# Optimization experiments

Hardware: AMD Instinct MI355X
Metric: run time of the kernel (lower is better)

The kernel has to match this reference:

```python
import jax, jax.numpy as jnp
import numpy as np

NUM_HEADS = 32
NUM_KV_HEADS = 8
HEAD_DIM = 128
HIDDEN = 4096
BLOCK_SIZE = 16
NUM_BLOCKS = 512
BLOCKS_PER_REQ = 256
B, S = 1, 2048
ROPE_BASE = 10000.0


def _rope_cos_sin(seq_len, dim, dtype):
    inv_freq = 1.0 / (ROPE_BASE ** (jnp.arange(0, dim, 2, dtype=jnp.float32) / dim))
    t = jnp.arange(seq_len, dtype=jnp.float32)
    freqs = jnp.outer(t, inv_freq)            # [S, dim/2]
    emb = jnp.concatenate([freqs, freqs], -1)  # [S, dim]
    return jnp.cos(emb).astype(dtype), jnp.sin(emb).astype(dtype)


def _rotate_half(x):
    d = x.shape[-1] // 2
    return jnp.concatenate([-x[..., d:], x[..., :d]], axis=-1)


def setup_inputs() -> dict:
    key = jax.random.key(0)
    ks = jax.random.split(key, 6)
    sc = 0.02
    return {
        "hidden_states": jax.random.normal(ks[0], (B, S, HIDDEN), jnp.float32),
        "k_cache": jax.random.normal(ks[1], (NUM_BLOCKS, NUM_KV_HEADS, BLOCK_SIZE, HEAD_DIM), jnp.float32),
        "v_cache": jax.random.normal(ks[2], (NUM_BLOCKS, NUM_KV_HEADS, BLOCK_SIZE, HEAD_DIM), jnp.float32),
        "Wq": jax.random.normal(ks[3], (HIDDEN, HIDDEN), jnp.float32) * sc,
        "Wo": jax.random.normal(ks[4], (HIDDEN, HIDDEN), jnp.float32) * sc,
        "block_table": jax.random.randint(ks[5], (BLOCKS_PER_REQ,), 0, NUM_BLOCKS, jnp.int32),
    }


def reference(hidden_states, k_cache, v_cache, Wq, Wo, block_table):
    Bq, Sq, D = hidden_states.shape
    # query projection + reshape to [B, H, S, d]
    q = (hidden_states @ Wq.T).reshape(Bq, Sq, NUM_HEADS, HEAD_DIM).transpose(0, 2, 1, 3)
    cos, sin = _rope_cos_sin(Sq, HEAD_DIM, q.dtype)  # [S, d]
    q = q * cos[None, None] + _rotate_half(q) * sin[None, None]

    # paged KV gather: [n_blk, kvH, blk, d] -> [kvH, kv_len, d]
    kv_len = BLOCKS_PER_REQ * BLOCK_SIZE
    K = k_cache[block_table].transpose(1, 0, 2, 3).reshape(NUM_KV_HEADS, kv_len, HEAD_DIM)
    V = v_cache[block_table].transpose(1, 0, 2, 3).reshape(NUM_KV_HEADS, kv_len, HEAD_DIM)

    # GQA: repeat_interleave kv heads to q heads
    factor = NUM_HEADS // NUM_KV_HEADS
    K = jnp.repeat(K, factor, axis=0)[None]  # [1, H, kv_len, d]
    V = jnp.repeat(V, factor, axis=0)[None]

    scores = jnp.einsum('bhsd,bhkd->bhsk', q, K) / jnp.sqrt(jnp.asarray(HEAD_DIM, q.dtype))
    attn = jax.nn.softmax(scores, axis=-1)
    ctx = jnp.einsum('bhsk,bhkd->bhsd', attn, V)
    ctx = ctx.transpose(0, 2, 1, 3).reshape(Bq, Sq, D)
    return ctx @ Wo.T
```

## Files before the change

### kernel.cpp

```cpp
#include <hip/hip_runtime.h>
#include <hip/hip_bf16.h>

typedef __bf16 bf16;
typedef __bf16 bf16x4 __attribute__((ext_vector_type(4)));
typedef __bf16 bf16x8 __attribute__((ext_vector_type(8)));
typedef float f32x4 __attribute__((ext_vector_type(4)));

#define AS1 __attribute__((address_space(1)))
#define AS3 __attribute__((address_space(3)))
#define GLD16(gptr, lptr) \
  __builtin_amdgcn_global_load_lds((const AS1 unsigned int*)(gptr), \
                                   (AS3 unsigned int*)(lptr), 16, 0, 0)

#define NUM_H   32
#define NUM_KVH 8
#define DH      128
#define SEQ     2048
#define KVLEN   4096
#define HID     4096
#define RSCALE  0.08838834764831845f

__global__ void prep_hs(const float* __restrict__ hs, bf16* __restrict__ out) {
  int tid = blockIdx.x * 256 + threadIdx.x;
  size_t o = (size_t)tid * 8;
  float4 a = *(const float4*)(hs + o);
  float4 b = *(const float4*)(hs + o + 4);
  bf16x8 w = {(bf16)a.x, (bf16)a.y, (bf16)a.z, (bf16)a.w,
              (bf16)b.x, (bf16)b.y, (bf16)b.z, (bf16)b.w};
  *(bf16x8*)(out + o) = w;
}

__global__ void prep_k(const float* __restrict__ kc, const int* __restrict__ bt,
                       bf16* __restrict__ Kg) {
  int tid = blockIdx.x * 256 + threadIdx.x;
  int c   = tid & 31;
  int j   = (tid >> 5) & 4095;
  int kvh = tid >> 17;
  int blk = bt[j >> 4];
  float4 v = *(const float4*)(kc + (((size_t)blk * NUM_KVH + kvh) * 16 + (j & 15)) * DH + c * 4);
  bf16x4 w = {(bf16)v.x, (bf16)v.y, (bf16)v.z, (bf16)v.w};
  *(bf16x4*)(Kg + ((size_t)kvh * KVLEN + j) * DH + c * 4) = w;
}

__global__ void prep_v(const float* __restrict__ vc, const int* __restrict__ bt,
                       bf16* __restrict__ Vt) {
  __shared__ bf16 T[32][136];
  int e2 = blockIdx.x & 127, kvh = blockIdx.x >> 7;
  int t = threadIdx.x;
#pragma unroll
  for (int i = 0; i < 4; i++) {
    int idx = i * 256 + t;
    int pg  = idx >> 9;
    int pos = (idx >> 5) & 15;
    int c4  = idx & 31;
    int blk = bt[e2 * 2 + pg];
    float4 v = *(const float4*)(vc + (((size_t)blk * NUM_KVH + kvh) * 16 + pos) * DH + c4 * 4);
    bf16x4 w = {(bf16)v.x, (bf16)v.y, (bf16)v.z, (bf16)v.w};
    *(bf16x4*)(&T[pg * 16 + pos][c4 * 4]) = w;
  }
  __syncthreads();
  int d = t & 127, jc = t >> 7;
  bf16 tmp[16];
#pragma unroll
  for (int j = 0; j < 16; j++) tmp[j] = T[jc * 16 + j][d];
  bf16* dst = Vt + ((size_t)kvh * DH + d) * KVLEN + e2 * 32 + jc * 16;
  *(bf16x8*)dst = *(bf16x8*)tmp;
  *(bf16x8*)(dst + 8) = *(bf16x8*)(tmp + 8);
}

template <typename CT>
__global__ __launch_bounds__(512, 2)
void gemm_bb(const bf16* __restrict__ A, const bf16* __restrict__ B,
             CT* __restrict__ C, int M, int N, int K) {
  __shared__ alignas(16) bf16 As[2][128 * 64];
  __shared__ alignas(16) bf16 Bs[2][256 * 64];
  const int nwg = gridDim.x;
  const int q8  = nwg >> 3;
  const int wg  = ((int)blockIdx.x & 7) * q8 + ((int)blockIdx.x >> 3);
  const int nb = N >> 8;
  const int bm = wg / nb;
  const int bn = wg % nb;
  const int t = threadIdx.x;
  const int lane = t & 63, wave = t >> 6;
  const int lid = lane & 15, quad = lane >> 4;
  const int wm = (wave >> 2) * 64, wn = (wave & 3) * 64;
  const bf16* Ab = A + (size_t)bm * 128 * K;
  const bf16* Bb = B + (size_t)bn * 256 * K;
  f32x4 acc[4][4] = {};

  auto stage = [&](int buf, int k0) {
#pragma unroll
    for (int i = 0; i < 2; i++) {
      int id = i * 512 + t;
      int row = id >> 3, c = id & 7;
      int gc = c ^ (row & 7);
      GLD16(Ab + (size_t)row * K + k0 + gc * 8, &As[buf][id * 8]);
    }
#pragma unroll
    for (int i = 0; i < 4; i++) {
      int id = i * 512 + t;
      int row = id >> 3, c = id & 7;
      int gc = c ^ (row & 7);
      GLD16(Bb + (size_t)row * K + k0 + gc * 8, &Bs[buf][id * 8]);
    }
  };
  auto compute = [&](int buf) {
#pragma unroll
    for (int kk = 0; kk < 2; kk++) {
      bf16x8 af[4], bfr[4];
#pragma unroll
      for (int i = 0; i < 4; i++) {
        int row = wm + i * 16 + lid;
        af[i] = *(const bf16x8*)(&As[buf][row * 64 + ((kk * 4 + quad) ^ (row & 7)) * 8]);
      }
#pragma unroll
      for (int j = 0; j < 4; j++) {
        int row = wn + j * 16 + lid;
        bfr[j] = *(const bf16x8*)(&Bs[buf][row * 64 + ((kk * 4 + quad) ^ (row & 7)) * 8]);
      }
#pragma unroll
      for (int i = 0; i < 4; i++)
#pragma unroll
        for (int j = 0; j < 4; j++)
          acc[i][j] = __builtin_amdgcn_mfma_f32_16x16x32_bf16(af[i], bfr[j], acc[i][j], 0, 0, 0);
    }
  };

  stage(0, 0);
  __syncthreads();

  int cur = 0;
#pragma unroll 1
  for (int k0 = 64; k0 < K; k0 += 64) {
    stage(cur ^ 1, k0);
    __builtin_amdgcn_sched_barrier(0);
    compute(cur);
    __syncthreads();
    cur ^= 1;
  }
  compute(cur);

#pragma unroll
  for (int i = 0; i < 4; i++)
#pragma unroll
    for (int j = 0; j < 4; j++)
#pragma unroll
      for (int r = 0; r < 4; r++) {
        int m = bm * 128 + wm + i * 16 + quad * 4 + r;
        int n = bn * 256 + wn + j * 16 + lid;
        C[(size_t)m * N + n] = (CT)acc[i][j][r];
      }
}

template <typename CT>
__global__ __launch_bounds__(512, 2)
void gemm_bt2(const bf16* __restrict__ A, const float* __restrict__ B,
              CT* __restrict__ C, int M, int N, int K) {
  __shared__ alignas(16) bf16 As[2][128 * 64];
  __shared__ alignas(16) bf16 Bs[2][256 * 64];
  const int nb = N >> 8;
  const int bm = (int)blockIdx.x / nb;
  const int bn = (int)blockIdx.x % nb;
  const int t = threadIdx.x;
  const int lane = t & 63, wave = t >> 6;
  const int lid = lane & 15, quad = lane >> 4;
  const int wm = (wave >> 2) * 64, wn = (wave & 3) * 64;
  const bf16*  Ab = A + (size_t)bm * 128 * K;
  const float* Bb = B + (size_t)bn * 256 * K;
  f32x4 acc[4][4] = {};
  float4 breg[4][2];

  auto issueA = [&](int buf, int k0) {
#pragma unroll
    for (int i = 0; i < 2; i++) {
      int id = i * 512 + t;
      int row = id >> 3, c = id & 7;
      int gc = c ^ (row & 7);
      GLD16(Ab + (size_t)row * K + k0 + gc * 8, &As[buf][id * 8]);
    }
  };
  auto loadB = [&](int k0) {
#pragma unroll
    for (int i = 0; i < 4; i++) {
      int id = i * 512 + t;
      int row = id >> 3, c = id & 7;
      const float* src = Bb + (size_t)row * K + k0 + c * 8;
      breg[i][0] = *(const float4*)(src);
      breg[i][1] = *(const float4*)(src + 4);
    }
  };
  auto writeB = [&](int buf) {
#pragma unroll
    for (int i = 0; i < 4; i++) {
      int id = i * 512 + t;
      int row = id >> 3, c = id & 7;
      int sc = c ^ (row & 7);
      float4 u = breg[i][0], v = breg[i][1];
      bf16x8 w = {(bf16)u.x, (bf16)u.y, (bf16)u.z, (bf16)u.w,
                  (bf16)v.x, (bf16)v.y, (bf16)v.z, (bf16)v.w};
      *(bf16x8*)(&Bs[buf][row * 64 + sc * 8]) = w;
    }
  };
  auto compute = [&](int buf) {
#pragma unroll
    for (int kk = 0; kk < 2; kk++) {
      bf16x8 af[4], bfr[4];
#pragma unroll
      for (int i = 0; i < 4; i++) {
        int row = wm + i * 16 + lid;
        af[i] = *(const bf16x8*)(&As[buf][row * 64 + ((kk * 4 + quad) ^ (row & 7)) * 8]);
      }
#pragma unroll
      for (int j = 0; j < 4; j++) {
        int row = wn + j * 16 + lid;
        bfr[j] = *(const bf16x8*)(&Bs[buf][row * 64 + ((kk * 4 + quad) ^ (row & 7)) * 8]);
      }
#pragma unroll
      for (int i = 0; i < 4; i++)
#pragma unroll
        for (int j = 0; j < 4; j++)
          acc[i][j] = __builtin_amdgcn_mfma_f32_16x16x32_bf16(af[i], bfr[j], acc[i][j], 0, 0, 0);
    }
  };

  issueA(0, 0);
  loadB(0);
  writeB(0);
  __syncthreads();

  int cur = 0;
#pragma unroll 1
  for (int k0 = 64; k0 < K; k0 += 64) {
    issueA(cur ^ 1, k0);
    loadB(k0);
    __builtin_amdgcn_sched_barrier(0);
    compute(cur);
    __builtin_amdgcn_sched_barrier(0);
    writeB(cur ^ 1);
    __syncthreads();
    cur ^= 1;
  }
  compute(cur);

#pragma unroll
  for (int i = 0; i < 4; i++)
#pragma unroll
    for (int j = 0; j < 4; j++)
#pragma unroll
      for (int r = 0; r < 4; r++) {
        int m = bm * 128 + wm + i * 16 + quad * 4 + r;
        int n = bn * 256 + wn + j * 16 + lid;
        C[(size_t)m * N + n] = (CT)acc[i][j][r];
      }
}

__global__ void rope_q(bf16* __restrict__ Q) {
  __shared__ float tcs[64], tsn[64];
  int s = blockIdx.x;
  int t = threadIdx.x;
  if (t < 64) {
    float freq = expf(-(float)t * (logf(10000.f) / 64.f));
    float sn, cs;
    sincosf((float)s * freq, &sn, &cs);
    tsn[t] = sn; tcs[t] = cs;
  }
  __syncthreads();
  int h = t >> 3, d0 = (t & 7) * 8;
  bf16* ptr = Q + (size_t)s * HID + h * DH;
  bf16x8 lo = *(bf16x8*)(ptr + d0);
  bf16x8 hi = *(bf16x8*)(ptr + 64 + d0);
  bf16x8 olo, ohi;
#pragma unroll
  for (int e = 0; e < 8; e++) {
    float cs = tcs[d0 + e], sn = tsn[d0 + e];
    float q0 = (float)lo[e], q1 = (float)hi[e];
    olo[e] = (bf16)((q0 * cs - q1 * sn) * RSCALE);
    ohi[e] = (bf16)((q1 * cs + q0 * sn) * RSCALE);
  }
  *(bf16x8*)(ptr + d0) = olo;
  *(bf16x8*)(ptr + 64 + d0) = ohi;
}

__global__ __launch_bounds__(256, 2)
void attn(bf16* __restrict__ Q,
          const bf16* __restrict__ Kg,
          const bf16* __restrict__ Vt) {
  __shared__ alignas(16) bf16 Ks[64 * 128];
  __shared__ alignas(16) bf16 Vs[128 * 64];
  __shared__ alignas(16) bf16 Ps[4][2][16 * 72];
  const int bid = ((int)blockIdx.x & 7) * 64 + ((int)blockIdx.x >> 3);
  const int h = bid >> 4, qt2 = bid & 15;
  const int kvh = h >> 2;
  const int t = threadIdx.x;
  const int wave = t >> 6, lane = t & 63;
  const int lid = lane & 15, quad = lane >> 4;

  bf16x8 qf[2][4];
#pragma unroll
  for (int x = 0; x < 2; x++) {
    const bf16* qb = Q + (size_t)(qt2 * 128 + x * 64 + wave * 16 + lid) * HID + h * DH;
#pragma unroll
    for (int kc = 0; kc < 4; kc++) qf[x][kc] = *(const bf16x8*)(qb + kc * 32 + quad * 8);
  }
  const bf16* Kh = Kg + (size_t)kvh * KVLEN * DH;
  const bf16* Vh = Vt + (size_t)kvh * DH * KVLEN;
  f32x4 acc_o[2][8] = {};
  f32x4 lsum[2] = {};
  const bf16 one = (bf16)1.0f;
  const bf16x8 ones = {one, one, one, one, one, one, one, one};

  for (int kv0 = 0; kv0 < KVLEN; kv0 += 64) {
    __syncthreads();
#pragma unroll
    for (int i = 0; i < 4; i++) {
      int id = i * 256 + t;
      int row = id >> 4, cs = id & 15;
      int gc = cs ^ (row & 7);
      GLD16(Kh + (size_t)(kv0 + row) * DH + gc * 8, Ks + id * 8);
    }
#pragma unroll
    for (int i = 0; i < 4; i++) {
      int id = i * 256 + t;
      int d = id >> 3, cs = id & 7;
      int gc = cs ^ (d & 7);
      GLD16(Vh + (size_t)d * KVLEN + kv0 + gc * 8, Vs + id * 8);
    }
    __syncthreads();

    f32x4 sv[2][4];
#pragma unroll
    for (int n = 0; n < 4; n++) {
      f32x4 s0 = {}, s1 = {};
      int row = n * 16 + lid;
#pragma unroll
      for (int kc = 0; kc < 4; kc++) {
        int cs = (kc * 4 + quad) ^ (row & 7);
        bf16x8 kf = *(const bf16x8*)(Ks + row * DH + cs * 8);
        s0 = __builtin_amdgcn_mfma_f32_16x16x32_bf16(qf[0][kc], kf, s0, 0, 0, 0);
        s1 = __builtin_amdgcn_mfma_f32_16x16x32_bf16(qf[1][kc], kf, s1, 0, 0, 0);
      }
      sv[0][n] = s0; sv[1][n] = s1;
    }

#pragma unroll
    for (int x = 0; x < 2; x++)
#pragma unroll
      for (int r = 0; r < 4; r++)
#pragma unroll
        for (int n = 0; n < 4; n++)
          Ps[wave][x][(quad * 4 + r) * 72 + n * 16 + lid] = (bf16)__expf(sv[x][n][r]);

    bf16x8 pf[2][2];
#pragma unroll
    for (int x = 0; x < 2; x++)
#pragma unroll
      for (int kvc = 0; kvc < 2; kvc++)
        pf[x][kvc] = *(const bf16x8*)(&Ps[wave][x][0] + lid * 72 + kvc * 32 + quad * 8);

#pragma unroll
    for (int x = 0; x < 2; x++) {
      lsum[x] = __builtin_amdgcn_mfma_f32_16x16x32_bf16(pf[x][0], ones, lsum[x], 0, 0, 0);
      lsum[x] = __builtin_amdgcn_mfma_f32_16x16x32_bf16(pf[x][1], ones, lsum[x], 0, 0, 0);
    }

#pragma unroll
    for (int dt = 0; dt < 8; dt++) {
      int d = dt * 16 + lid;
#pragma unroll
      for (int kvc = 0; kvc < 2; kvc++) {
        int cs = (kvc * 4 + quad) ^ (d & 7);
        bf16x8 vf = *(const bf16x8*)(Vs + d * 64 + cs * 8);
        acc_o[0][dt] = __builtin_amdgcn_mfma_f32_16x16x32_bf16(pf[0][kvc], vf, acc_o[0][dt], 0, 0, 0);
        acc_o[1][dt] = __builtin_amdgcn_mfma_f32_16x16x32_bf16(pf[1][kvc], vf, acc_o[1][dt], 0, 0, 0);
      }
    }
  }

#pragma unroll
  for (int x = 0; x < 2; x++) {
    float rinv[4];
#pragma unroll
    for (int r = 0; r < 4; r++) rinv[r] = 1.0f / lsum[x][r];
#pragma unroll
    for (int dt = 0; dt < 8; dt++)
#pragma unroll
      for (int r = 0; r < 4; r++) {
        int m = qt2 * 128 + x * 64 + wave * 16 + quad * 4 + r;
        Q[(size_t)m * HID + h * DH + dt * 16 + lid] = (bf16)(acc_o[x][dt][r] * rinv[r]);
      }
  }
}

extern "C" void kernel_launch(void* const* d_in, const int* in_sizes, int n_in,
                              void* d_out, int out_size, void* d_ws, size_t ws_size,
                              hipStream_t stream) {
  const float* hs  = (const float*)d_in[0];
  const float* kca = (const float*)d_in[1];
  const float* vca = (const float*)d_in[2];
  const float* Wq  = (const float*)d_in[3];
  const float* Wo  = (const float*)d_in[4];
  const int*   bt  = (const int*)d_in[5];
  float* out = (float*)d_out;

  bf16* Qlin  = (bf16*)d_ws;
  bf16* Kg    = (bf16*)d_out;
  bf16* Vt    = (bf16*)((char*)d_out + (8u << 20));
  bf16* hs_bf = (bf16*)((char*)d_out + (16u << 20));

  prep_k<<<4096, 256, 0, stream>>>(kca, bt, Kg);
  prep_v<<<1024, 256, 0, stream>>>(vca, bt, Vt);
  prep_hs<<<4096, 256, 0, stream>>>(hs, hs_bf);

  if (ws_size >= (80u << 20)) {
    bf16* Wq_bf = (bf16*)((char*)d_ws + (16u << 20));
    bf16* Wo_bf = (bf16*)((char*)d_ws + (48u << 20));
    prep_hs<<<8192, 256, 0, stream>>>(Wq, Wq_bf);
    prep_hs<<<8192, 256, 0, stream>>>(Wo, Wo_bf);
    gemm_bb<bf16><<<256, 512, 0, stream>>>(hs_bf, Wq_bf, Qlin, SEQ, HID, HID);
    rope_q<<<SEQ, 256, 0, stream>>>(Qlin);
    attn<<<512, 256, 0, stream>>>(Qlin, Kg, Vt);
    gemm_bb<float><<<256, 512, 0, stream>>>(Qlin, Wo_bf, out, SEQ, HID, HID);
  } else {
    gemm_bt2<bf16><<<256, 512, 0, stream>>>(hs_bf, Wq, Qlin, SEQ, HID, HID);
    rope_q<<<SEQ, 256, 0, stream>>>(Qlin);
    attn<<<512, 256, 0, stream>>>(Qlin, Kg, Vt);
    gemm_bt2<float><<<256, 512, 0, stream>>>(Qlin, Wo, out, SEQ, HID, HID);
  }
}
```

Measured before the change: 558.7 us.

## Shrink GEMM tiles, double-buffer attention KV, swap MFMA operands for vector stores

Result: faster. 522.9 us (-6.4%).

```diff
diff --git a/kernel.cpp b/kernel.cpp
--- a/kernel.cpp
+++ b/kernel.cpp
@@ -69,36 +69,36 @@
 }
 
 template <typename CT>
-__global__ __launch_bounds__(512, 2)
+__global__ __launch_bounds__(256, 2)
 void gemm_bb(const bf16* __restrict__ A, const bf16* __restrict__ B,
              CT* __restrict__ C, int M, int N, int K) {
   __shared__ alignas(16) bf16 As[2][128 * 64];
-  __shared__ alignas(16) bf16 Bs[2][256 * 64];
+  __shared__ alignas(16) bf16 Bs[2][128 * 64];
   const int nwg = gridDim.x;
   const int q8  = nwg >> 3;
   const int wg  = ((int)blockIdx.x & 7) * q8 + ((int)blockIdx.x >> 3);
-  const int nb = N >> 8;
+  const int nb = N >> 7;
   const int bm = wg / nb;
   const int bn = wg % nb;
   const int t = threadIdx.x;
   const int lane = t & 63, wave = t >> 6;
   const int lid = lane & 15, quad = lane >> 4;
-  const int wm = (wave >> 2) * 64, wn = (wave & 3) * 64;
+  const int wm = (wave >> 1) * 64, wn = (wave & 1) * 64;
   const bf16* Ab = A + (size_t)bm * 128 * K;
-  const bf16* Bb = B + (size_t)bn * 256 * K;
+  const bf16* Bb = B + (size_t)bn * 128 * K;
   f32x4 acc[4][4] = {};
 
   auto stage = [&](int buf, int k0) {
 #pragma unroll
-    for (int i = 0; i < 2; i++) {
-      int id = i * 512 + t;
+    for (int i = 0; i < 4; i++) {
+      int id = i * 256 + t;
       int row = id >> 3, c = id & 7;
       int gc = c ^ (row & 7);
       GLD16(Ab + (size_t)row * K + k0 + gc * 8, &As[buf][id * 8]);
     }
 #pragma unroll
     for (int i = 0; i < 4; i++) {
-      int id = i * 512 + t;
+      int id = i * 256 + t;
       int row = id >> 3, c = id & 7;
       int gc = c ^ (row & 7);
       GLD16(Bb + (size_t)row * K + k0 + gc * 8, &Bs[buf][id * 8]);
@@ -122,7 +122,7 @@
       for (int i = 0; i < 4; i++)
 #pragma unroll
         for (int j = 0; j < 4; j++)
-          acc[i][j] = __builtin_amdgcn_mfma_f32_16x16x32_bf16(af[i], bfr[j], acc[i][j], 0, 0, 0);
+          acc[i][j] = __builtin_amdgcn_mfma_f32_16x16x32_bf16(bfr[j], af[i], acc[i][j], 0, 0, 0);
     }
   };
 
@@ -143,13 +143,168 @@
 #pragma unroll
   for (int i = 0; i < 4; i++)
 #pragma unroll
-    for (int j = 0; j < 4; j++)
-#pragma unroll
-      for (int r = 0; r < 4; r++) {
-        int m = bm * 128 + wm + i * 16 + quad * 4 + r;
-        int n = bn * 256 + wn + j * 16 + lid;
-        C[(size_t)m * N + n] = (CT)acc[i][j][r];
-      }
+    for (int j = 0; j < 4; j++) {
+      int m = bm * 128 + wm + i * 16 + lid;
+      int n = bn * 128 + wn + j * 16 + quad * 4;
+      if constexpr (sizeof(CT) == 4) {
+        float4 w = {acc[i][j][0], acc[i][j][1], acc[i][j][2], acc[i][j][3]};
+        *(float4*)(&C[(size_t)m * N + n]) = w;
+      } else {
+        bf16x4 w = {(bf16)acc[i][j][0], (bf16)acc[i][j][1],
+                    (bf16)acc[i][j][2], (bf16)acc[i][j][3]};
+        *(bf16x4*)(&C[(size_t)m * N + n]) = w;
+      }
+    }
+}
+
+__global__ void rope_q(bf16* __restrict__ Q) {
+  __shared__ float tcs[64], tsn[64];
+  int s = blockIdx.x;
+  int t = threadIdx.x;
+  if (t < 64) {
+    float freq = expf(-(float)t * (logf(10000.f) / 64.f));
+    float sn, cs;
+    sincosf((float)s * freq, &sn, &cs);
+    tsn[t] = sn; tcs[t] = cs;
+  }
+  __syncthreads();
+  int h = t >> 3, d0 = (t & 7) * 8;
+  bf16* ptr = Q + (size_t)s * HID + h * DH;
+  bf16x8 lo = *(bf16x8*)(ptr + d0);
+  bf16x8 hi = *(bf16x8*)(ptr + 64 + d0);
+  bf16x8 olo, ohi;
+#pragma unroll
+  for (int e = 0; e < 8; e++) {
+    float cs = tcs[d0 + e], sn = tsn[d0 + e];
+    float q0 = (float)lo[e], q1 = (float)hi[e];
+    olo[e] = (bf16)((q0 * cs - q1 * sn) * RSCALE);
+    ohi[e] = (bf16)((q1 * cs + q0 * sn) * RSCALE);
+  }
+  *(bf16x8*)(ptr + d0) = olo;
+  *(bf16x8*)(ptr + 64 + d0) = ohi;
+}
+
+__global__ __launch_bounds__(256, 2)
+void attn(bf16* __restrict__ Q,
+          const bf16* __restrict__ Kg,
+          const bf16* __restrict__ Vt) {
+  __shared__ alignas(16) bf16 Ks[2][64 * 128];
+  __shared__ alignas(16) bf16 Vs[2][128 * 64];
+  __shared__ alignas(16) bf16 Ps[4][2][1024];
+  const int bid = ((int)blockIdx.x & 7) * 64 + ((int)blockIdx.x >> 3);
+  const int h = bid >> 4, qt2 = bid & 15;
+  const int kvh = h >> 2;
+  const int t = threadIdx.x;
+  const int wave = t >> 6, lane = t & 63;
+  const int lid = lane & 15, quad = lane >> 4;
+
+  bf16x8 qf[2][4];
+#pragma unroll
+  for (int x = 0; x < 2; x++) {
+    const bf16* qb = Q + (size_t)(qt2 * 128 + x * 64 + wave * 16 + lid) * HID + h * DH;
+#pragma unroll
+    for (int kc = 0; kc < 4; kc++) qf[x][kc] = *(const bf16x8*)(qb + kc * 32 + quad * 8);
+  }
+  const bf16* Kh = Kg + (size_t)kvh * KVLEN * DH;
+  const bf16* Vh = Vt + (size_t)kvh * DH * KVLEN;
+  f32x4 acc_o[2][8] = {};
+  f32x4 lsum[2] = {};
+  const bf16 one = (bf16)1.0f;
+  const bf16x8 ones = {one, one, one, one, one, one, one, one};
+
+  auto stage = [&](int buf, int kv0) {
+#pragma unroll
+    for (int i = 0; i < 4; i++) {
+      int id = i * 256 + t;
+      int row = id >> 4, cs = id & 15;
+      int gc = cs ^ (row & 7);
+      GLD16(Kh + (size_t)(kv0 + row) * DH + gc * 8, &Ks[buf][id * 8]);
+    }
+#pragma unroll
+    for (int i = 0; i < 4; i++) {
+      int id = i * 256 + t;
+      int d = id >> 3, cs = id & 7;
+      int gc = cs ^ (d & 7);
+      GLD16(Vh + (size_t)d * KVLEN + kv0 + gc * 8, &Vs[buf][id * 8]);
+    }
+  };
+
+  stage(0, 0);
+  __syncthreads();
+
+  int cur = 0;
+#pragma unroll 1
+  for (int kv0 = 0; kv0 < KVLEN; kv0 += 64) {
+    if (kv0 + 64 < KVLEN) stage(cur ^ 1, kv0 + 64);
+    __builtin_amdgcn_sched_barrier(0);
+
+    f32x4 sv[2][4];
+#pragma unroll
+    for (int n = 0; n < 4; n++) {
+      f32x4 s0 = {}, s1 = {};
+      int row = n * 16 + lid;
+#pragma unroll
+      for (int kc = 0; kc < 4; kc++) {
+        int cs = (kc * 4 + quad) ^ (row & 7);
+        bf16x8 kf = *(const bf16x8*)(&Ks[cur][row * DH + cs * 8]);
+        s0 = __builtin_amdgcn_mfma_f32_16x16x32_bf16(kf, qf[0][kc], s0, 0, 0, 0);
+        s1 = __builtin_amdgcn_mfma_f32_16x16x32_bf16(kf, qf[1][kc], s1, 0, 0, 0);
+      }
+      sv[0][n] = s0; sv[1][n] = s1;
+    }
+
+#pragma unroll
+    for (int x = 0; x < 2; x++)
+#pragma unroll
+      for (int n = 0; n < 4; n++) {
+        bf16x4 w = {(bf16)__expf(sv[x][n][0]), (bf16)__expf(sv[x][n][1]),
+                    (bf16)__expf(sv[x][n][2]), (bf16)__expf(sv[x][n][3])};
+        int c = (2 * n + (quad >> 1)) ^ (lid & 7);
+        *(bf16x4*)(&Ps[wave][x][lid * 64 + c * 8 + (quad & 1) * 4]) = w;
+      }
+
+    bf16x8 pf[2][2];
+#pragma unroll
+    for (int x = 0; x < 2; x++)
+#pragma unroll
+      for (int kvc = 0; kvc < 2; kvc++) {
+        int c = (kvc * 4 + quad) ^ (lid & 7);
+        pf[x][kvc] = *(const bf16x8*)(&Ps[wave][x][lid * 64 + c * 8]);
+      }
+
+#pragma unroll
+    for (int x = 0; x < 2; x++) {
+      lsum[x] = __builtin_amdgcn_mfma_f32_16x16x32_bf16(ones, pf[x][0], lsum[x], 0, 0, 0);
+      lsum[x] = __builtin_amdgcn_mfma_f32_16x16x32_bf16(ones, pf[x][1], lsum[x], 0, 0, 0);
+    }
+
+#pragma unroll
+    for (int dt = 0; dt < 8; dt++) {
+      int d = dt * 16 + lid;
+#pragma unroll
+      for (int kvc = 0; kvc < 2; kvc++) {
+        int cs = (kvc * 4 + quad) ^ (d & 7);
+        bf16x8 vf = *(const bf16x8*)(&Vs[cur][d * 64 + cs * 8]);
+        acc_o[0][dt] = __builtin_amdgcn_mfma_f32_16x16x32_bf16(vf, pf[0][kvc], acc_o[0][dt], 0, 0, 0);
+        acc_o[1][dt] = __builtin_amdgcn_mfma_f32_16x16x32_bf16(vf, pf[1][kvc], acc_o[1][dt], 0, 0, 0);
+      }
+    }
+
+    __syncthreads();
+    cur ^= 1;
+  }
+
+#pragma unroll
+  for (int x = 0; x < 2; x++) {
+    float rinv = 1.0f / lsum[x][0];
+    int q = qt2 * 128 + x * 64 + wave * 16 + lid;
+#pragma unroll
+    for (int dt = 0; dt < 8; dt++) {
+      bf16x4 w = {(bf16)(acc_o[x][dt][0] * rinv), (bf16)(acc_o[x][dt][1] * rinv),
+                  (bf16)(acc_o[x][dt][2] * rinv), (bf16)(acc_o[x][dt][3] * rinv)};
+      *(bf16x4*)(&Q[(size_t)q * HID + h * DH + dt * 16 + quad * 4]) = w;
+    }
+  }
 }
 
 template <typename CT>
@@ -254,143 +409,6 @@
       }
 }
 
-__global__ void rope_q(bf16* __restrict__ Q) {
-  __shared__ float tcs[64], tsn[64];
-  int s = blockIdx.x;
-  int t = threadIdx.x;
-  if (t < 64) {
-    float freq = expf(-(float)t * (logf(10000.f) / 64.f));
-    float sn, cs;
-    sincosf((float)s * freq, &sn, &cs);
-    tsn[t] = sn; tcs[t] = cs;
-  }
-  __syncthreads();
-  int h = t >> 3, d0 = (t & 7) * 8;
-  bf16* ptr = Q + (size_t)s * HID + h * DH;
-  bf16x8 lo = *(bf16x8*)(ptr + d0);
-  bf16x8 hi = *(bf16x8*)(ptr + 64 + d0);
-  bf16x8 olo, ohi;
-#pragma unroll
-  for (int e = 0; e < 8; e++) {
-    float cs = tcs[d0 + e], sn = tsn[d0 + e];
-    float q0 = (float)lo[e], q1 = (float)hi[e];
-    olo[e] = (bf16)((q0 * cs - q1 * sn) * RSCALE);
-    ohi[e] = (bf16)((q1 * cs + q0 * sn) * RSCALE);
-  }
-  *(bf16x8*)(ptr + d0) = olo;
-  *(bf16x8*)(ptr + 64 + d0) = ohi;
-}
-
-__global__ __launch_bounds__(256, 2)
-void attn(bf16* __restrict__ Q,
-          const bf16* __restrict__ Kg,
-          const bf16* __restrict__ Vt) {
-  __shared__ alignas(16) bf16 Ks[64 * 128];
-  __shared__ alignas(16) bf16 Vs[128 * 64];
-  __shared__ alignas(16) bf16 Ps[4][2][16 * 72];
-  const int bid = ((int)blockIdx.x & 7) * 64 + ((int)blockIdx.x >> 3);
-  const int h = bid >> 4, qt2 = bid & 15;
-  const int kvh = h >> 2;
-  const int t = threadIdx.x;
-  const int wave = t >> 6, lane = t & 63;
-  const int lid = lane & 15, quad = lane >> 4;
-
-  bf16x8 qf[2][4];
-#pragma unroll
-  for (int x = 0; x < 2; x++) {
-    const bf16* qb = Q + (size_t)(qt2 * 128 + x * 64 + wave * 16 + lid) * HID + h * DH;
-#pragma unroll
-    for (int kc = 0; kc < 4; kc++) qf[x][kc] = *(const bf16x8*)(qb + kc * 32 + quad * 8);
-  }
-  const bf16* Kh = Kg + (size_t)kvh * KVLEN * DH;
-  const bf16* Vh = Vt + (size_t)kvh * DH * KVLEN;
-  f32x4 acc_o[2][8] = {};
-  f32x4 lsum[2] = {};
-  const bf16 one = (bf16)1.0f;
-  const bf16x8 ones = {one, one, one, one, one, one, one, one};
-
-  for (int kv0 = 0; kv0 < KVLEN; kv0 += 64) {
-    __syncthreads();
-#pragma unroll
-    for (int i = 0; i < 4; i++) {
-      int id = i * 256 + t;
-      int row = id >> 4, cs = id & 15;
-      int gc = cs ^ (row & 7);
-      GLD16(Kh + (size_t)(kv0 + row) * DH + gc * 8, Ks + id * 8);
-    }
-#pragma unroll
-    for (int i = 0; i < 4; i++) {
-      int id = i * 256 + t;
-      int d = id >> 3, cs = id & 7;
-      int gc = cs ^ (d & 7);
-      GLD16(Vh + (size_t)d * KVLEN + kv0 + gc * 8, Vs + id * 8);
-    }
-    __syncthreads();
-
-    f32x4 sv[2][4];
-#pragma unroll
-    for (int n = 0; n < 4; n++) {
-      f32x4 s0 = {}, s1 = {};
-      int row = n * 16 + lid;
-#pragma unroll
-      for (int kc = 0; kc < 4; kc++) {
-        int cs = (kc * 4 + quad) ^ (row & 7);
-        bf16x8 kf = *(const bf16x8*)(Ks + row * DH + cs * 8);
-        s0 = __builtin_amdgcn_mfma_f32_16x16x32_bf16(qf[0][kc], kf, s0, 0, 0, 0);
-        s1 = __builtin_amdgcn_mfma_f32_16x16x32_bf16(qf[1][kc], kf, s1, 0, 0, 0);
-      }
-      sv[0][n] = s0; sv[1][n] = s1;
-    }
-
-#pragma unroll
-    for (int x = 0; x < 2; x++)
-#pragma unroll
-      for (int r = 0; r < 4; r++)
-#pragma unroll
-        for (int n = 0; n < 4; n++)
-          Ps[wave][x][(quad * 4 + r) * 72 + n * 16 + lid] = (bf16)__expf(sv[x][n][r]);
-
-    bf16x8 pf[2][2];
-#pragma unroll
-    for (int x = 0; x < 2; x++)
-#pragma unroll
-      for (int kvc = 0; kvc < 2; kvc++)
-        pf[x][kvc] = *(const bf16x8*)(&Ps[wave][x][0] + lid * 72 + kvc * 32 + quad * 8);
-
-#pragma unroll
-    for (int x = 0; x < 2; x++) {
-      lsum[x] = __builtin_amdgcn_mfma_f32_16x16x32_bf16(pf[x][0], ones, lsum[x], 0, 0, 0);
-      lsum[x] = __builtin_amdgcn_mfma_f32_16x16x32_bf16(pf[x][1], ones, lsum[x], 0, 0, 0);
-    }
-
-#pragma unroll
-    for (int dt = 0; dt < 8; dt++) {
-      int d = dt * 16 + lid;
-#pragma unroll
-      for (int kvc = 0; kvc < 2; kvc++) {
-        int cs = (kvc * 4 + quad) ^ (d & 7);
-        bf16x8 vf = *(const bf16x8*)(Vs + d * 64 + cs * 8);
-        acc_o[0][dt] = __builtin_amdgcn_mfma_f32_16x16x32_bf16(pf[0][kvc], vf, acc_o[0][dt], 0, 0, 0);
-        acc_o[1][dt] = __builtin_amdgcn_mfma_f32_16x16x32_bf16(pf[1][kvc], vf, acc_o[1][dt], 0, 0, 0);
-      }
-    }
-  }
-
-#pragma unroll
-  for (int x = 0; x < 2; x++) {
-    float rinv[4];
-#pragma unroll
-    for (int r = 0; r < 4; r++) rinv[r] = 1.0f / lsum[x][r];
-#pragma unroll
-    for (int dt = 0; dt < 8; dt++)
-#pragma unroll
-      for (int r = 0; r < 4; r++) {
-        int m = qt2 * 128 + x * 64 + wave * 16 + quad * 4 + r;
-        Q[(size_t)m * HID + h * DH + dt * 16 + lid] = (bf16)(acc_o[x][dt][r] * rinv[r]);
-      }
-  }
-}
-
 extern "C" void kernel_launch(void* const* d_in, const int* in_sizes, int n_in,
                               void* d_out, int out_size, void* d_ws, size_t ws_size,
                               hipStream_t stream) {
@@ -416,10 +434,10 @@
     bf16* Wo_bf = (bf16*)((char*)d_ws + (48u << 20));
     prep_hs<<<8192, 256, 0, stream>>>(Wq, Wq_bf);
     prep_hs<<<8192, 256, 0, stream>>>(Wo, Wo_bf);
-    gemm_bb<bf16><<<256, 512, 0, stream>>>(hs_bf, Wq_bf, Qlin, SEQ, HID, HID);
+    gemm_bb<bf16><<<512, 256, 0, stream>>>(hs_bf, Wq_bf, Qlin, SEQ, HID, HID);
     rope_q<<<SEQ, 256, 0, stream>>>(Qlin);
     attn<<<512, 256, 0, stream>>>(Qlin, Kg, Vt);
-    gemm_bb<float><<<256, 512, 0, stream>>>(Qlin, Wo_bf, out, SEQ, HID, HID);
+    gemm_bb<float><<<512, 256, 0, stream>>>(Qlin, Wo_bf, out, SEQ, HID, HID);
   } else {
     gemm_bt2<bf16><<<256, 512, 0, stream>>>(hs_bf, Wq, Qlin, SEQ, HID, HID);
     rope_q<<<SEQ, 256, 0, stream>>>(Qlin);
```
